# Optimization experiments

Hardware: AMD Instinct MI355X
Metric: run time of the kernel (lower is better)

## Reference

```python
import jax, jax.numpy as jnp
from jax import lax
import numpy as np

B, T = 512, 20
RES, C3D, AUD, P, H, NC = 2048, 4096, 128, 1024, 1024, 200


def setup_inputs() -> dict:
    key = jax.random.key(0)
    ks = jax.random.split(key, 40)

    def n(k, shape, s=0.02):
        return jax.random.normal(k, shape, jnp.float32) * s

    inp = {
        "resnet_features": jax.random.normal(ks[0], (B, T, RES), jnp.float32),
        "c3d_features": jax.random.normal(ks[1], (B, T, C3D), jnp.float32),
        "audio_features": jax.random.normal(ks[2], (B, T, AUD), jnp.float32),
        "W_audio": n(ks[3], (P, AUD)), "b_audio": jnp.zeros((P,), jnp.float32),
        "W_resnet": n(ks[4], (P, RES)), "b_resnet": jnp.zeros((P,), jnp.float32),
        "W_c3d": n(ks[5], (P, C3D)), "b_c3d": jnp.zeros((P,), jnp.float32),
    }
    i = 6
    for nm in ["audio_fwd", "audio_rev", "resnet_fwd", "resnet_rev", "c3d_fwd", "c3d_rev"]:
        inp[nm + "_Wih"] = n(ks[i], (4 * H, P)); i += 1
        inp[nm + "_Whh"] = n(ks[i], (4 * H, H)); i += 1
        inp[nm + "_bih"] = jnp.zeros((4 * H,), jnp.float32)
        inp[nm + "_bhh"] = jnp.zeros((4 * H,), jnp.float32)
    inp["W_out"] = n(ks[i], (NC, 2 * H)); i += 1
    inp["b_out"] = jnp.zeros((NC,), jnp.float32)
    return inp


def _run_lstm(xs, Wih, Whh, bih, bhh, reverse):
    # xs: (B, T, P). PyTorch LSTMCell gate order: i, f, g, o.
    b = bih + bhh

    def step(carry, x):
        h, c = carry
        gates = x @ Wih.T + h @ Whh.T + b  # (B, 4H)
        i, f, g, o = jnp.split(gates, 4, axis=-1)
        c = jax.nn.sigmoid(f) * c + jax.nn.sigmoid(i) * jnp.tanh(g)
        h = jax.nn.sigmoid(o) * jnp.tanh(c)
        return (h, c), None

    bsz = xs.shape[0]
    init = (jnp.zeros((bsz, H), xs.dtype), jnp.zeros((bsz, H), xs.dtype))
    (h, c), _ = lax.scan(step, init, jnp.swapaxes(xs, 0, 1), reverse=reverse)
    return h


def reference(resnet_features, c3d_features, audio_features, W_audio, b_audio, W_resnet, b_resnet, W_c3d, b_c3d, audio_fwd_Wih, audio_fwd_Whh, audio_fwd_bih, audio_fwd_bhh, audio_rev_Wih, audio_rev_Whh, audio_rev_bih, audio_rev_bhh, resnet_fwd_Wih, resnet_fwd_Whh, resnet_fwd_bih, resnet_fwd_bhh, resnet_rev_Wih, resnet_rev_Whh, resnet_rev_bih, resnet_rev_bhh, c3d_fwd_Wih, c3d_fwd_Whh, c3d_fwd_bih, c3d_fwd_bhh, c3d_rev_Wih, c3d_rev_Whh, c3d_rev_bih, c3d_rev_bhh, W_out, b_out):
    # Dropouts are identity in eval mode.
    out_a = audio_features @ W_audio.T + b_audio    # (B, T, P)
    out_r = resnet_features @ W_resnet.T + b_resnet
    out_c = c3d_features @ W_c3d.T + b_c3d

    h_af = _run_lstm(out_a, audio_fwd_Wih, audio_fwd_Whh, audio_fwd_bih, audio_fwd_bhh, False)
    h_ar = _run_lstm(out_a, audio_rev_Wih, audio_rev_Whh, audio_rev_bih, audio_rev_bhh, True)
    h_rf = _run_lstm(out_r, resnet_fwd_Wih, resnet_fwd_Whh, resnet_fwd_bih, resnet_fwd_bhh, False)
    h_rr = _run_lstm(out_r, resnet_rev_Wih, resnet_rev_Whh, resnet_rev_bih, resnet_rev_bhh, True)
    h_cf = _run_lstm(out_c, c3d_fwd_Wih, c3d_fwd_Whh, c3d_fwd_bih, c3d_fwd_bhh, False)
    h_cr = _run_lstm(out_c, c3d_rev_Wih, c3d_rev_Whh, c3d_rev_bih, c3d_rev_bhh, True)

    audio_final = jnp.concatenate([h_af, h_ar], axis=1)
    resnet_final = jnp.concatenate([h_rf, h_rr], axis=1)
    c3d_final = jnp.concatenate([h_cf, h_cr], axis=1)
    fused = audio_final * resnet_final * c3d_final  # (B, 2H)
    return fused @ W_out.T + b_out  # (B, NC)
```

## Files before the change

### kernel.cpp

```cpp
#include <hip/hip_runtime.h>
#include <cstdio>
#include <cstdint>

#define TT    20
#define BATCH 512
#define HID   1024
#define G4    4096
#define NG    8192
#define BT    (BATCH * TT)
#define NCLS  200
#define SH    ((size_t)BATCH * HID)

typedef unsigned short u16;
typedef __attribute__((ext_vector_type(8))) short short8;
typedef __attribute__((ext_vector_type(4))) float f32x4;
typedef __attribute__((ext_vector_type(4))) unsigned short u16x4;

__device__ __forceinline__ float sigf(float x) { return 1.0f / (1.0f + __expf(-x)); }

__device__ __forceinline__ u16 f2bf(float x) {
    unsigned u = __float_as_uint(x);
    u += 0x7FFFu + ((u >> 16) & 1u);
    return (u16)(u >> 16);
}
__device__ __forceinline__ float bf2f(u16 b) { return __uint_as_float(((unsigned)b) << 16); }

__device__ __forceinline__ void gld16(const u16* g, u16* l) {
    __builtin_amdgcn_global_load_lds(
        (const __attribute__((address_space(1))) void*)g,
        (__attribute__((address_space(3))) void*)l, 16, 0, 0);
}

__global__ void cvt4_kernel(const float* __restrict__ x, u16* __restrict__ y, int n4)
{
    const int stride = gridDim.x * blockDim.x;
    for (int i = blockIdx.x * blockDim.x + threadIdx.x; i < n4; i += stride) {
        const float4 v = ((const float4*)x)[i];
        uint2 hp;
        hp.x = (unsigned)f2bf(v.x) | ((unsigned)f2bf(v.y) << 16);
        hp.y = (unsigned)f2bf(v.z) | ((unsigned)f2bf(v.w) << 16);
        ((uint2*)y)[i] = hp;
    }
}

struct CvtJob { const float* src; u16* dst; };
struct CvtBatch { CvtJob j[6]; };
__global__ void cvt4_batch(CvtBatch cb, int n4)
{
    const float* __restrict__ x = cb.j[blockIdx.y].src;
    u16* __restrict__ y = cb.j[blockIdx.y].dst;
    const int stride = gridDim.x * blockDim.x;
    for (int i = blockIdx.x * blockDim.x + threadIdx.x; i < n4; i += stride) {
        const float4 v = ((const float4*)x)[i];
        uint2 hp;
        hp.x = (unsigned)f2bf(v.x) | ((unsigned)f2bf(v.y) << 16);
        hp.y = (unsigned)f2bf(v.z) | ((unsigned)f2bf(v.w) << 16);
        ((uint2*)y)[i] = hp;
    }
}

__global__ void cvtperm_audio(const float* __restrict__ in, u16* __restrict__ out)
{
    const int tid4 = blockIdx.x * blockDim.x + threadIdx.x;
    if (tid4 >= BT * 128 / 4) return;
    const int row = tid4 >> 5;
    const int kk  = (tid4 & 31) << 2;
    const int t = row % 20, b = row / 20;
    const float4 v = *(const float4*)(in + (size_t)row * 128 + kk);
    uint2 hp;
    hp.x = (unsigned)f2bf(v.x) | ((unsigned)f2bf(v.y) << 16);
    hp.y = (unsigned)f2bf(v.z) | ((unsigned)f2bf(v.w) << 16);
    *(uint2*)(out + (size_t)(t * 512 + b) * 128 + kk) = hp;
}

__global__ void transpose_cvt(const float* __restrict__ in, u16* __restrict__ out)
{
    const int idx = blockIdx.x * blockDim.x + threadIdx.x;
    if (idx >= 128 * 1024) return;
    const int a = idx >> 10, p = idx & 1023;
    out[idx] = f2bf(in[p * 128 + a]);
}

__global__ void bvec_kernel(const float* __restrict__ Wih0, const float* __restrict__ Wih1,
                            const float* __restrict__ ba,
                            const float* __restrict__ bi0, const float* __restrict__ bh0,
                            const float* __restrict__ bi1, const float* __restrict__ bh1,
                            float* __restrict__ bvec)
{
    const int wv = blockIdx.x * 4 + (threadIdx.x >> 6);
    const int lane = threadIdx.x & 63;
    const float* Wrow = (wv < 4096) ? Wih0 + (size_t)wv * 1024
                                    : Wih1 + (size_t)(wv - 4096) * 1024;
    float s = 0.f;
#pragma unroll
    for (int c = 0; c < 4; ++c) {
        const float4 w = *(const float4*)(Wrow + c * 256 + lane * 4);
        const float4 x = *(const float4*)(ba + c * 256 + lane * 4);
        s += w.x * x.x + w.y * x.y + w.z * x.z + w.w * x.w;
    }
#pragma unroll
    for (int o = 32; o; o >>= 1) s += __shfl_xor(s, o);
    if (lane == 0) {
        const int n = wv & 4095;
        bvec[wv] = s + ((wv < 4096) ? bi0[n] + bh0[n] : bi1[n] + bh1[n]);
    }
}

__global__ void bias_cat_kernel(const float* __restrict__ bi0, const float* __restrict__ bh0,
                                const float* __restrict__ bi1, const float* __restrict__ bh1,
                                float* __restrict__ bcat)
{
    const int n = blockIdx.x * blockDim.x + threadIdx.x;
    if (n >= NG) return;
    bcat[n] = (n < G4) ? (bi0[n] + bh0[n]) : (bi1[n - G4] + bh1[n - G4]);
}

template<int MODE>
__launch_bounds__(256)
__global__ void gemm_b16(const u16* __restrict__ A, const u16* __restrict__ W,
                         const float* __restrict__ b1, u16* __restrict__ Cb,
                         int M, int N, int K, int cm)
{
    __shared__ u16 sA[4][128][8]; __shared__ u16 sW[4][128][8];
    const int tid = threadIdx.x, lane = tid & 63, w = tid >> 6;
    const int wr = w >> 1, wc = w & 1;

    const int nwg = gridDim.x;
    const int cpx = nwg >> 3;
    const int lg = (blockIdx.x & 7) * cpx + (blockIdx.x >> 3);
    const int nby = N >> 7;
    const int cb = cm * nby;
    const int chunk = lg / cb;
    const int r = lg - chunk * cb;
    const int m0 = (chunk * cm + (r % cm)) * 128;
    const int n0 = (r / cm) * 128;

    const u16* A0 = A + (size_t)m0 * K;
    const u16* W0 = W + (size_t)n0 * K;

    f32x4 acc[4][4];
#pragma unroll
    for (int i = 0; i < 4; ++i)
#pragma unroll
        for (int j = 0; j < 4; ++j) acc[i][j] = f32x4{0.f, 0.f, 0.f, 0.f};

    const int u1 = tid, u2 = tid + 256;
    const size_t go1 = (size_t)(u1 & 127) * K + (u1 >> 7) * 8;
    const size_t go2 = (size_t)(u2 & 127) * K + (u2 >> 7) * 8;
    u16* const l1 = (u16*)sA + (size_t)u1 * 8;
    u16* const l2 = (u16*)sA + (size_t)u2 * 8;
    const size_t dW = (u16*)sW - (u16*)sA;

    for (int k0 = 0; k0 < K; k0 += 32) {
        gld16(A0 + go1 + k0, l1);       gld16(A0 + go2 + k0, l2);
        gld16(W0 + go1 + k0, l1 + dW);  gld16(W0 + go2 + k0, l2 + dW);
        __syncthreads();

        const int kb = lane >> 4, rr = lane & 15;
        short8 Av[4], Wv[4];
#pragma unroll
        for (int i = 0; i < 4; ++i) {
            Av[i] = *(const short8*)&sA[kb][wr * 64 + i * 16 + rr][0];
            Wv[i] = *(const short8*)&sW[kb][wc * 64 + i * 16 + rr][0];
        }
#pragma unroll
        for (int i = 0; i < 4; ++i)
#pragma unroll
            for (int j = 0; j < 4; ++j)
                acc[i][j] = __builtin_amdgcn_mfma_f32_16x16x32_bf16(Av[i], Wv[j], acc[i][j], 0, 0, 0);
        __syncthreads();
    }

    const int rr = lane & 15, rg = lane >> 4;
#pragma unroll
    for (int j = 0; j < 4; ++j) {
        const int col = n0 + wc * 64 + j * 16 + rr;
        const float bias = b1 ? b1[col] : 0.f;
#pragma unroll
        for (int i = 0; i < 4; ++i) {
            if (MODE == 1) {
                u16x4 pk;
#pragma unroll
                for (int q = 0; q < 4; ++q) pk[q] = f2bf(acc[i][j][q] + bias);
                const int grp = (m0 >> 2) + wr * 16 + i * 4 + rg;
                __builtin_nontemporal_store(pk, (u16x4*)(Cb + ((size_t)grp * N + col) * 4));
            } else if (MODE == 0) {
#pragma unroll
                for (int q = 0; q < 4; ++q) {
                    const int row = m0 + wr * 64 + i * 16 + rg * 4 + q;
                    const int rowp = (row % 20) * 512 + row / 20;
                    Cb[(size_t)rowp * N + col] = f2bf(acc[i][j][q] + bias);
                }
            } else {
#pragma unroll
                for (int q = 0; q < 4; ++q) {
                    const int row = m0 + wr * 64 + i * 16 + rg * 4 + q;
                    Cb[(size_t)row * N + col] = f2bf(acc[i][j][q] + bias);
                }
            }
        }
    }
}

__launch_bounds__(256)
__global__ void lstm_step6(const u16* __restrict__ whhAll,
                           const u16* __restrict__ Gall,
                           const u16* __restrict__ hinAll,
                           u16* __restrict__ houtAll,
                           float* __restrict__ cbAll,
                           float* __restrict__ hfinAll,
                           int s, int write_hfin)
{
    const int l = blockIdx.z;
    __shared__ u16 sA[2][4][64][8];
    __shared__ u16 sW[2][4][128][8];
    const int tid = threadIdx.x, lane = tid & 63, w = tid >> 6;
    const int wr = w >> 1, wc = w & 1;
    const int j0 = blockIdx.x * 32;
    const int m0 = blockIdx.y * 64;

    const u16* __restrict__ hin = hinAll + (size_t)l * SH;
    const u16* __restrict__ Whh = whhAll + (size_t)l * G4 * HID;
    const int do_gemm = (s > 0);

    f32x4 acc[2][4];
#pragma unroll
    for (int i = 0; i < 2; ++i)
#pragma unroll
        for (int g = 0; g < 4; ++g) acc[i][g] = f32x4{0.f, 0.f, 0.f, 0.f};

    const int rr = lane & 15, rg = lane >> 4;

    if (do_gemm) {
        const size_t goA = (size_t)(m0 + (tid & 63)) * HID + (tid >> 6) * 8;
        const int rW = tid & 127;
        const int wrow = ((rW >> 4) & 3) * HID + j0 + (rW >> 6) * 16 + (rW & 15);
        const size_t goW1 = (size_t)wrow * HID + (tid >> 7) * 8;
        const size_t goW2 = (size_t)wrow * HID + ((tid >> 7) + 2) * 8;
        u16* const ldA  = (u16*)sA + (size_t)tid * 8;
        u16* const ldW1 = (u16*)sW + (size_t)tid * 8;
        u16* const ldW2 = (u16*)sW + (size_t)(tid + 256) * 8;

        gld16(hin + goA,  ldA);
        gld16(Whh + goW1, ldW1);
        gld16(Whh + goW2, ldW2);
        __syncthreads();

        for (int k0 = 0; k0 < HID; k0 += 32) {
            const int bf = (k0 >> 5) & 1;
            if (k0 + 32 < HID) {
                gld16(hin + goA  + k0 + 32, ldA  + (bf ^ 1) * 2048);
                gld16(Whh + goW1 + k0 + 32, ldW1 + (bf ^ 1) * 4096);
                gld16(Whh + goW2 + k0 + 32, ldW2 + (bf ^ 1) * 4096);
            }
            const int kb = lane >> 4;
            short8 Av[2], Wv[4];
#pragma unroll
            for (int i = 0; i < 2; ++i)
                Av[i] = *(const short8*)&sA[bf][kb][wr * 32 + i * 16 + rr][0];
#pragma unroll
            for (int g = 0; g < 4; ++g)
                Wv[g] = *(const short8*)&sW[bf][kb][wc * 64 + g * 16 + rr][0];
#pragma unroll
            for (int i = 0; i < 2; ++i)
#pragma unroll
                for (int g = 0; g < 4; ++g)
                    acc[i][g] = __builtin_amdgcn_mfma_f32_16x16x32_bf16(Av[i], Wv[g], acc[i][g], 0, 0, 0);
            __syncthreads();
        }
    }

    const int j = j0 + wc * 16 + rr;
    const int t = (l & 1) ? (TT - 1 - s) : s;
    const u16* __restrict__ Gl = Gall + (size_t)(l >> 1) * BT * NG;
    const int cbase = (l & 1) * G4 + j;
    float* __restrict__ cb = cbAll + (size_t)l * SH;
    float* __restrict__ hf = hfinAll + (size_t)l * SH;
    u16* __restrict__ ho = houtAll + (size_t)l * SH;
#pragma unroll
    for (int i = 0; i < 2; ++i) {
        const int grp = t * 128 + (m0 >> 2) + wr * 8 + i * 4 + rg;
        const u16* gb = Gl + (size_t)grp * NG * 4;
        const u16x4 g0 = __builtin_nontemporal_load((const u16x4*)(gb + (size_t)cbase * 4));
        const u16x4 g1 = __builtin_nontemporal_load((const u16x4*)(gb + (size_t)(cbase + 1024) * 4));
        const u16x4 g2 = __builtin_nontemporal_load((const u16x4*)(gb + (size_t)(cbase + 2048) * 4));
        const u16x4 g3 = __builtin_nontemporal_load((const u16x4*)(gb + (size_t)(cbase + 3072) * 4));
#pragma unroll
        for (int q = 0; q < 4; ++q) {
            const int b = m0 + wr * 32 + i * 16 + rg * 4 + q;
            const float pi = acc[i][0][q] + bf2f(g0[q]);
            const float pf = acc[i][1][q] + bf2f(g1[q]);
            const float pg = acc[i][2][q] + bf2f(g2[q]);
            const float po = acc[i][3][q] + bf2f(g3[q]);
            const size_t idx = (size_t)b * HID + j;
            const float cprev = do_gemm ? cb[idx] : 0.f;
            const float cn = sigf(pf) * cprev + sigf(pi) * tanhf(pg);
            cb[idx] = cn;
            const float h = sigf(po) * tanhf(cn);
            if (write_hfin) hf[idx] = h;
            else            ho[idx] = f2bf(h);
        }
    }
}

__global__ void fuse_mul_kernel(const float* __restrict__ hfin, float* __restrict__ fused)
{
    const int idx = blockIdx.x * blockDim.x + threadIdx.x;
    if (idx >= BATCH * 2 * HID) return;
    const int b = idx >> 11;
    const int n = idx & 2047;
    const int half = n >> 10;
    const int j = n & 1023;
    const size_t o = (size_t)b * HID + j;
    fused[idx] = hfin[(size_t)(0 + half) * SH + o] *
                 hfin[(size_t)(2 + half) * SH + o] *
                 hfin[(size_t)(4 + half) * SH + o];
}

__launch_bounds__(256)
__global__ void gemm_bias_kernel(const float* __restrict__ A, const float* __restrict__ W,
                                 const float* __restrict__ b1,
                                 float* __restrict__ C, int M, int N, int K)
{
    __shared__ float As[16][68];
    __shared__ float Ws[16][68];
    const int tid = threadIdx.x;
    const int tx = tid & 15, ty = tid >> 4;
    const int m0 = blockIdx.x * 64;
    const int n0 = blockIdx.y * 64;
    const int lr = tid >> 2;
    const int lk = (tid & 3) << 2;
    const bool mok = (m0 + lr < M);
    const bool nok = (n0 + lr < N);
    const float* Arow = A + (size_t)(m0 + lr) * K + lk;
    const float* Wrow = W + (size_t)(n0 + lr) * K + lk;
    float acc[4][4] = {};

    for (int k0 = 0; k0 < K; k0 += 16) {
        float4 av = make_float4(0.f, 0.f, 0.f, 0.f);
        float4 wv = make_float4(0.f, 0.f, 0.f, 0.f);
        if (mok) av = *(const float4*)(Arow + k0);
        if (nok) wv = *(const float4*)(Wrow + k0);
        As[lk + 0][lr] = av.x; As[lk + 1][lr] = av.y; As[lk + 2][lr] = av.z; As[lk + 3][lr] = av.w;
        Ws[lk + 0][lr] = wv.x; Ws[lk + 1][lr] = wv.y; Ws[lk + 2][lr] = wv.z; Ws[lk + 3][lr] = wv.w;
        __syncthreads();
#pragma unroll
        for (int k = 0; k < 16; ++k) {
            const float4 a = *(const float4*)&As[k][ty << 2];
            const float4 ww = *(const float4*)&Ws[k][tx << 2];
            const float a4[4] = {a.x, a.y, a.z, a.w};
            const float w4[4] = {ww.x, ww.y, ww.z, ww.w};
#pragma unroll
            for (int i = 0; i < 4; ++i)
#pragma unroll
                for (int j = 0; j < 4; ++j)
                    acc[i][j] = fmaf(a4[i], w4[j], acc[i][j]);
        }
        __syncthreads();
    }

#pragma unroll
    for (int i = 0; i < 4; ++i) {
        const int m = m0 + (ty << 2) + i;
        if (m >= M) continue;
#pragma unroll
        for (int j = 0; j < 4; ++j) {
            const int n = n0 + (tx << 2) + j;
            if (n >= N) continue;
            C[(size_t)m * N + n] = acc[i][j] + (b1 ? b1[n] : 0.f);
        }
    }
}

extern "C" void kernel_launch(void* const* d_in, const int* in_sizes, int n_in,
                              void* d_out, int out_size, void* d_ws, size_t ws_size,
                              hipStream_t stream)
{
    const float* resnet   = (const float*)d_in[0];
    const float* c3d      = (const float*)d_in[1];
    const float* audio    = (const float*)d_in[2];
    const float* W_audio  = (const float*)d_in[3];
    const float* b_audio  = (const float*)d_in[4];
    const float* W_resnet = (const float*)d_in[5];
    const float* b_resnet = (const float*)d_in[6];
    const float* W_c3d    = (const float*)d_in[7];
    const float* b_c3d    = (const float*)d_in[8];
    const float* Wih[6]; const float* Whh[6]; const float* bih[6]; const float* bhh[6];
    for (int l = 0; l < 6; ++l) {
        Wih[l] = (const float*)d_in[9 + 4 * l];
        Whh[l] = (const float*)d_in[10 + 4 * l];
        bih[l] = (const float*)d_in[11 + 4 * l];
        bhh[l] = (const float*)d_in[12 + 4 * l];
    }
    const float* W_out = (const float*)d_in[33];
    const float* b_out = (const float*)d_in[34];
    float* out = (float*)d_out;

    const float* feat[3] = { audio, resnet, c3d };
    const float* fw[3]   = { W_audio, W_resnet, W_c3d };
    const float* fb[3]   = { b_audio, b_resnet, b_c3d };
    const int    fK[3]   = { 128, 2048, 4096 };

    char* p = (char*)d_ws;
    char* pend = p + ws_size;
    auto alloc = [&](size_t bytes) -> void* {
        void* q = p; p += (bytes + 255) & ~(size_t)255; return q;
    };
    const size_t FW = (size_t)1024 * (128 + 2048 + 4096);
    u16* Gall  = (u16*)alloc((size_t)3 * BT * NG * 2);
    u16* featB = Gall + (size_t)2 * BT * NG;
    u16* fwB   = (u16*)alloc(FW * 2);
    u16* wihB  = (u16*)alloc((size_t)NG * HID * 2);
    u16* whhB  = (u16*)alloc((size_t)3 * NG * HID * 2);
    u16* projB = (u16*)alloc((size_t)BT * HID * 2);
    float* bcat = (float*)alloc((size_t)NG * 4);
    u16* hA    = (u16*)alloc((size_t)6 * SH * 2);
    u16* hB    = (u16*)alloc((size_t)6 * SH * 2);
    float* cb    = (float*)alloc((size_t)6 * SH * 4);
    float* hfin  = (float*)alloc((size_t)6 * SH * 4);
    float* fused = (float*)alloc((size_t)BATCH * 2 * HID * 4);
    u16* waT      = (u16*)alloc((size_t)128 * 1024 * 2);
    u16* wcombB   = (u16*)alloc((size_t)NG * 128 * 2);
    u16* featPerm = (u16*)alloc((size_t)BT * 128 * 2);
    float* bvec   = (float*)alloc((size_t)NG * 4);
    if (p > pend) {
        fprintf(stderr, "kernel_launch: ws too small: need %zu have %zu\n",
                (size_t)(p - (char*)d_ws), ws_size);
        return;
    }

    const dim3 blk(256);
    const size_t fwOff[3] = { 0, (size_t)1024 * 128, (size_t)1024 * 128 + (size_t)1024 * 2048 };
    const int n4w = (G4 * HID) / 4;

    for (int st = 1; st < 3; ++st) {
        const int n4 = (1024 * fK[st]) / 4;
        cvt4_kernel<<<dim3(min(2048, (n4 + 255) / 256)), blk, 0, stream>>>(
            fw[st], fwB + fwOff[st], n4);
    }
    {
        CvtBatch b6;
        for (int l = 0; l < 6; ++l) { b6.j[l].src = Whh[l]; b6.j[l].dst = whhB + (size_t)l * G4 * HID; }
        cvt4_batch<<<dim3(768, 6), blk, 0, stream>>>(b6, n4w);
    }

    {
        CvtBatch b2;
        for (int d = 0; d < 2; ++d) { b2.j[d].src = Wih[d]; b2.j[d].dst = wihB + (size_t)d * G4 * HID; }
        cvt4_batch<<<dim3(768, 2), blk, 0, stream>>>(b2, n4w);
        transpose_cvt<<<dim3(512), blk, 0, stream>>>(W_audio, waT);
        gemm_b16<2><<<dim3(64), blk, 0, stream>>>(wihB, waT, nullptr, wcombB, NG, 128, 1024, 8);
        bvec_kernel<<<dim3(2048), blk, 0, stream>>>(
            Wih[0], Wih[1], b_audio, bih[0], bhh[0], bih[1], bhh[1], bvec);
        cvtperm_audio<<<dim3((BT * 128 / 4 + 255) / 256), blk, 0, stream>>>(audio, featPerm);
        gemm_b16<1><<<dim3((BT / 128) * (NG / 128)), blk, 0, stream>>>(
            featPerm, wcombB, bvec, Gall, BT, NG, 128, 8);
    }

    for (int st = 1; st < 3; ++st) {
        const int K = fK[st];
        cvt4_kernel<<<dim3(2048), blk, 0, stream>>>(feat[st], featB, (BT * K) / 4);
        gemm_b16<0><<<dim3((BT / 128) * (HID / 128)), blk, 0, stream>>>(
            featB, fwB + fwOff[st], fb[st], projB, BT, HID, K, 8);
        {
            CvtBatch b2;
            for (int d = 0; d < 2; ++d) {
                b2.j[d].src = Wih[st * 2 + d];
                b2.j[d].dst = wihB + (size_t)d * G4 * HID;
            }
            cvt4_batch<<<dim3(768, 2), blk, 0, stream>>>(b2, n4w);
        }
        bias_cat_kernel<<<dim3(NG / 256), blk, 0, stream>>>(
            bih[st * 2], bhh[st * 2], bih[st * 2 + 1], bhh[st * 2 + 1], bcat);
        gemm_b16<1><<<dim3((BT / 128) * (NG / 128)), blk, 0, stream>>>(
            projB, wihB, bcat, Gall + (size_t)st * BT * NG, BT, NG, HID, 8);
    }

    for (int s = 0; s < TT; ++s) {
        const u16* in = (s & 1) ? hB : hA;
        u16*      o  = (s & 1) ? hA : hB;
        lstm_step6<<<dim3(HID / 32, BATCH / 64, 6), blk, 0, stream>>>(
            whhB, Gall, in, o, cb, hfin, s, s == TT - 1 ? 1 : 0);
    }

    fuse_mul_kernel<<<dim3((BATCH * 2 * HID) / 256), blk, 0, stream>>>(hfin, fused);

    gemm_bias_kernel<<<dim3(BATCH / 64, (NCLS + 63) / 64), blk, 0, stream>>>(
        fused, W_out, b_out, out, BATCH, NCLS, 2 * HID);
}
```

Baseline: 3.084 ms.

## Fuse fp32-to-bf16 feature conversion into projection GEMM and double-buffer LDS tiles

The projection GEMM now reads fp32 features directly and converts them to bf16 while staging into shared memory, removing the separate conversion kernel and its intermediate buffer round trip. The GEMM also gains a two-stage shared-memory double buffer so the next K tile is loaded while the current one is multiplied. The fused fp32 load path uses synchronous register staging, which may stall, and LDS usage doubles.

```diff
diff --git a/kernel.cpp b/kernel.cpp
--- a/kernel.cpp
+++ b/kernel.cpp
@@ -115,13 +115,15 @@
     bcat[n] = (n < G4) ? (bi0[n] + bh0[n]) : (bi1[n - G4] + bh1[n - G4]);
 }
 
-template<int MODE>
+template<int MODE, bool AFP32>
 __launch_bounds__(256)
-__global__ void gemm_b16(const u16* __restrict__ A, const u16* __restrict__ W,
+__global__ void gemm_b16(const u16* __restrict__ A, const float* __restrict__ Af,
+                         const u16* __restrict__ W,
                          const float* __restrict__ b1, u16* __restrict__ Cb,
                          int M, int N, int K, int cm)
 {
-    __shared__ u16 sA[4][128][8]; __shared__ u16 sW[4][128][8];
+    __shared__ u16 sA[2][4][128][8];
+    __shared__ u16 sW[2][4][128][8];
     const int tid = threadIdx.x, lane = tid & 63, w = tid >> 6;
     const int wr = w >> 1, wc = w & 1;
 
@@ -135,8 +137,9 @@
     const int m0 = (chunk * cm + (r % cm)) * 128;
     const int n0 = (r / cm) * 128;
 
-    const u16* A0 = A + (size_t)m0 * K;
-    const u16* W0 = W + (size_t)n0 * K;
+    const u16*   A0  = AFP32 ? nullptr : A + (size_t)m0 * K;
+    const float* A0f = AFP32 ? Af + (size_t)m0 * K : nullptr;
+    const u16*   W0  = W + (size_t)n0 * K;
 
     f32x4 acc[4][4];
 #pragma unroll
@@ -147,21 +150,48 @@
     const int u1 = tid, u2 = tid + 256;
     const size_t go1 = (size_t)(u1 & 127) * K + (u1 >> 7) * 8;
     const size_t go2 = (size_t)(u2 & 127) * K + (u2 >> 7) * 8;
-    u16* const l1 = (u16*)sA + (size_t)u1 * 8;
-    u16* const l2 = (u16*)sA + (size_t)u2 * 8;
-    const size_t dW = (u16*)sW - (u16*)sA;
+    u16* const ldA1 = (u16*)sA + (size_t)u1 * 8;
+    u16* const ldA2 = (u16*)sA + (size_t)u2 * 8;
+    u16* const ldW1 = (u16*)sW + (size_t)u1 * 8;
+    u16* const ldW2 = (u16*)sW + (size_t)u2 * 8;
+
+    auto stageA = [&](int kk, int buf) {
+        if (AFP32) {
+            const float4 x0 = *(const float4*)(A0f + go1 + kk);
+            const float4 x1 = *(const float4*)(A0f + go1 + kk + 4);
+            const float4 y0 = *(const float4*)(A0f + go2 + kk);
+            const float4 y1 = *(const float4*)(A0f + go2 + kk + 4);
+            u16 hb[8];
+            hb[0] = f2bf(x0.x); hb[1] = f2bf(x0.y); hb[2] = f2bf(x0.z); hb[3] = f2bf(x0.w);
+            hb[4] = f2bf(x1.x); hb[5] = f2bf(x1.y); hb[6] = f2bf(x1.z); hb[7] = f2bf(x1.w);
+            *(uint4*)(ldA1 + buf * 4096) = *(uint4*)hb;
+            hb[0] = f2bf(y0.x); hb[1] = f2bf(y0.y); hb[2] = f2bf(y0.z); hb[3] = f2bf(y0.w);
+            hb[4] = f2bf(y1.x); hb[5] = f2bf(y1.y); hb[6] = f2bf(y1.z); hb[7] = f2bf(y1.w);
+            *(uint4*)(ldA2 + buf * 4096) = *(uint4*)hb;
+        } else {
+            gld16(A0 + go1 + kk, ldA1 + buf * 4096);
+            gld16(A0 + go2 + kk, ldA2 + buf * 4096);
+        }
+    };
+
+    stageA(0, 0);
+    gld16(W0 + go1, ldW1);
+    gld16(W0 + go2, ldW2);
+    __syncthreads();
 
     for (int k0 = 0; k0 < K; k0 += 32) {
-        gld16(A0 + go1 + k0, l1);       gld16(A0 + go2 + k0, l2);
-        gld16(W0 + go1 + k0, l1 + dW);  gld16(W0 + go2 + k0, l2 + dW);
-        __syncthreads();
-
+        const int bf = (k0 >> 5) & 1;
+        if (k0 + 32 < K) {
+            stageA(k0 + 32, bf ^ 1);
+            gld16(W0 + go1 + k0 + 32, ldW1 + (bf ^ 1) * 4096);
+            gld16(W0 + go2 + k0 + 32, ldW2 + (bf ^ 1) * 4096);
+        }
         const int kb = lane >> 4, rr = lane & 15;
         short8 Av[4], Wv[4];
 #pragma unroll
         for (int i = 0; i < 4; ++i) {
-            Av[i] = *(const short8*)&sA[kb][wr * 64 + i * 16 + rr][0];
-            Wv[i] = *(const short8*)&sW[kb][wc * 64 + i * 16 + rr][0];
+            Av[i] = *(const short8*)&sA[bf][kb][wr * 64 + i * 16 + rr][0];
+            Wv[i] = *(const short8*)&sW[bf][kb][wc * 64 + i * 16 + rr][0];
         }
 #pragma unroll
         for (int i = 0; i < 4; ++i)
@@ -408,7 +438,6 @@
     };
     const size_t FW = (size_t)1024 * (128 + 2048 + 4096);
     u16* Gall  = (u16*)alloc((size_t)3 * BT * NG * 2);
-    u16* featB = Gall + (size_t)2 * BT * NG;
     u16* fwB   = (u16*)alloc(FW * 2);
     u16* wihB  = (u16*)alloc((size_t)NG * HID * 2);
     u16* whhB  = (u16*)alloc((size_t)3 * NG * HID * 2);
@@ -449,19 +478,19 @@
         for (int d = 0; d < 2; ++d) { b2.j[d].src = Wih[d]; b2.j[d].dst = wihB + (size_t)d * G4 * HID; }
         cvt4_batch<<<dim3(768, 2), blk, 0, stream>>>(b2, n4w);
         transpose_cvt<<<dim3(512), blk, 0, stream>>>(W_audio, waT);
-        gemm_b16<2><<<dim3(64), blk, 0, stream>>>(wihB, waT, nullptr, wcombB, NG, 128, 1024, 8);
+        gemm_b16<2, false><<<dim3(64), blk, 0, stream>>>(
+            wihB, nullptr, waT, nullptr, wcombB, NG, 128, 1024, 8);
         bvec_kernel<<<dim3(2048), blk, 0, stream>>>(
             Wih[0], Wih[1], b_audio, bih[0], bhh[0], bih[1], bhh[1], bvec);
         cvtperm_audio<<<dim3((BT * 128 / 4 + 255) / 256), blk, 0, stream>>>(audio, featPerm);
-        gemm_b16<1><<<dim3((BT / 128) * (NG / 128)), blk, 0, stream>>>(
-            featPerm, wcombB, bvec, Gall, BT, NG, 128, 8);
+        gemm_b16<1, false><<<dim3((BT / 128) * (NG / 128)), blk, 0, stream>>>(
+            featPerm, nullptr, wcombB, bvec, Gall, BT, NG, 128, 8);
     }
 
     for (int st = 1; st < 3; ++st) {
         const int K = fK[st];
-        cvt4_kernel<<<dim3(2048), blk, 0, stream>>>(feat[st], featB, (BT * K) / 4);
-        gemm_b16<0><<<dim3((BT / 128) * (HID / 128)), blk, 0, stream>>>(
-            featB, fwB + fwOff[st], fb[st], projB, BT, HID, K, 8);
+        gemm_b16<0, true><<<dim3((BT / 128) * (HID / 128)), blk, 0, stream>>>(
+            nullptr, feat[st], fwB + fwOff[st], fb[st], projB, BT, HID, K, 8);
         {
             CvtBatch b2;
             for (int d = 0; d < 2; ++d) {
@@ -472,8 +501,8 @@
         }
         bias_cat_kernel<<<dim3(NG / 256), blk, 0, stream>>>(
             bih[st * 2], bhh[st * 2], bih[st * 2 + 1], bhh[st * 2 + 1], bcat);
-        gemm_b16<1><<<dim3((BT / 128) * (NG / 128)), blk, 0, stream>>>(
-            projB, wihB, bcat, Gall + (size_t)st * BT * NG, BT, NG, HID, 8);
+        gemm_b16<1, false><<<dim3((BT / 128) * (NG / 128)), blk, 0, stream>>>(
+            projB, nullptr, wihB, bcat, Gall + (size_t)st * BT * NG, BT, NG, HID, 8);
     }
 
     for (int s = 0; s < TT; ++s) {
```

Measured after the change: 3.220 ms. 4.4% more time.
